# Performance work log

Hardware: AMD Instinct MI355X
Metric: run time of the kernel (lower is better)

Reference implementation:

```python
import jax, jax.numpy as jnp
import numpy as np

N_NODES = 50000
N_EDGES = 800000
D_IN = 128
H = 4
F = 16


def setup_inputs() -> dict:
    key = jax.random.key(0)
    k1, k2, k3, k4 = jax.random.split(key, 4)
    feat = jax.random.normal(k1, (N_NODES, D_IN), dtype=jnp.float32)
    W = jax.random.normal(k2, (D_IN, H * F), dtype=jnp.float32) / np.sqrt(D_IN)
    src = jax.random.randint(k3, (N_EDGES,), 0, N_NODES, dtype=jnp.int32)
    dst = jax.random.randint(k4, (N_EDGES,), 0, N_NODES, dtype=jnp.int32)
    return {"feat": feat, "W": W, "src": src, "dst": dst}


def reference(feat, W, src, dst):
    # Project: [N, D_in] @ [D_in, H*F] -> [N, H, F]
    ft = (feat @ W).reshape(N_NODES, H, F)
    # Per-edge dot-product scores, scaled: [E, H]
    e = jnp.einsum('ehf,ehf->eh', ft[src], ft[dst]) / np.sqrt(F).astype(np.float32)
    # Segment (per-destination) softmax over incoming edges
    seg_max = jax.ops.segment_max(e, dst, num_segments=N_NODES)  # [N, H]
    ex = jnp.exp(e - seg_max[dst])
    denom = jax.ops.segment_sum(ex, dst, num_segments=N_NODES)  # [N, H]
    sa = ex / denom[dst]  # [E, H]
    # Weighted scatter-sum of source features: [N, H, F]
    msgs = ft[src] * sa[:, :, None]
    out = jax.ops.segment_sum(msgs, dst, num_segments=N_NODES)
    return out
```

## Files before the change

kernel.cpp:

```cpp
#include <hip/hip_runtime.h>
#include <hip/hip_fp16.h>

#define N_NODES 50000
#define N_EDGES 800000
#define D_IN 128
#define HH 4
#define FF 16
#define HF 64
#define NBUCKETS 196
#define BCAP 4608
#define CHUNK 2048
#define NBIN_BLOCKS ((N_EDGES + CHUNK - 1) / CHUNK)
#define GEMM_BLOCKS ((N_NODES + 63) / 64)

struct __align__(8) Half4 { __half2 a, b; };

__global__ __launch_bounds__(256, 2) void gemm_kernel(const float* __restrict__ feat,
                                                      const float* __restrict__ W,
                                                      __half* __restrict__ fth) {
    __shared__ float As[64][132];
    __shared__ float Bs[D_IN][HF];

    {
        const float4* W4 = (const float4*)W;
        float4* B4 = (float4*)Bs;
#pragma unroll
        for (int i = 0; i < 8; ++i) {
            int idx = threadIdx.x + 256 * i;
            B4[idx] = W4[idx];
        }
    }
    {
        int row0 = blockIdx.x * 64;
        const float4* F4 = (const float4*)feat;
#pragma unroll
        for (int i = 0; i < 8; ++i) {
            int idx = threadIdx.x + 256 * i;
            int r = idx >> 5;
            int c4 = idx & 31;
            float4 v = make_float4(0.f, 0.f, 0.f, 0.f);
            int row = row0 + r;
            if (row < N_NODES) v = F4[(size_t)row * 32 + c4];
            *(float4*)&As[r][c4 * 4] = v;
        }
    }
    __syncthreads();

    const int tr = threadIdx.x >> 4;
    const int tc = threadIdx.x & 15;

    float acc[4][4] = {};
#pragma unroll 8
    for (int k = 0; k < D_IN; k += 4) {
        float av[4][4], bv[4][4];
#pragma unroll
        for (int i = 0; i < 4; ++i) {
            float4 a = *(const float4*)&As[tr * 4 + i][k];
            av[i][0] = a.x; av[i][1] = a.y; av[i][2] = a.z; av[i][3] = a.w;
        }
#pragma unroll
        for (int j = 0; j < 4; ++j) {
            float4 b = *(const float4*)&Bs[k + j][tc * 4];
            bv[j][0] = b.x; bv[j][1] = b.y; bv[j][2] = b.z; bv[j][3] = b.w;
        }
#pragma unroll
        for (int i = 0; i < 4; ++i)
#pragma unroll
            for (int j = 0; j < 4; ++j)
#pragma unroll
                for (int c = 0; c < 4; ++c)
                    acc[i][c] = fmaf(av[i][j], bv[j][c], acc[i][c]);
    }

    int row0 = blockIdx.x * 64;
#pragma unroll
    for (int i = 0; i < 4; ++i) {
        int row = row0 + tr * 4 + i;
        if (row < N_NODES) {
            Half4 h;
            h.a = __floats2half2_rn(acc[i][0], acc[i][1]);
            h.b = __floats2half2_rn(acc[i][2], acc[i][3]);
            *(Half4*)&fth[(size_t)row * HF + tc * 4] = h;
        }
    }
}

__global__ __launch_bounds__(256) void bin_kernel(const int* __restrict__ src,
                                                  const int* __restrict__ dst,
                                                  int* __restrict__ gcur,
                                                  int* __restrict__ recs) {
    __shared__ int hist[256];
    __shared__ int offs[256];
    __shared__ int cur[256];
    __shared__ int lrec[CHUNK];

    int tid = threadIdx.x;
    int e0 = blockIdx.x * CHUNK;
    int n = N_EDGES - e0; if (n > CHUNK) n = CHUNK;

    hist[tid] = 0;
    __syncthreads();

    int myrec[CHUNK / 256];
    int myb[CHUNK / 256];
#pragma unroll
    for (int k = 0; k < CHUNK / 256; ++k) {
        int idx = tid + k * 256;
        myb[k] = -1;
        if (idx < n) {
            int s = src[e0 + idx];
            int d = dst[e0 + idx];
            int b = d >> 8;
            myrec[k] = s | ((d & 255) << 16);
            myb[k] = b;
            atomicAdd(&hist[b], 1);
        }
    }
    __syncthreads();

    int val = hist[tid];
    offs[tid] = val;
    __syncthreads();
#pragma unroll
    for (int off = 1; off < 256; off <<= 1) {
        int t = (tid >= off) ? offs[tid - off] : 0;
        __syncthreads();
        offs[tid] += t;
        __syncthreads();
    }
    int excl = offs[tid] - val;
    __syncthreads();
    offs[tid] = excl;
    cur[tid] = excl;
    __syncthreads();

#pragma unroll
    for (int k = 0; k < CHUNK / 256; ++k) {
        if (myb[k] >= 0) {
            int p = atomicAdd(&cur[myb[k]], 1);
            lrec[p] = myrec[k];
        }
    }
    __syncthreads();

    if (tid < NBUCKETS) {
        int c = hist[tid];
        if (c > 0) {
            int g = atomicAdd(&gcur[tid], c);
            if (g + c > BCAP) c = (BCAP > g) ? (BCAP - g) : 0;
            int lo = offs[tid];
            int* dp = recs + (size_t)tid * BCAP + g;
            for (int i = 0; i < c; ++i) dp[i] = lrec[lo + i];
        }
    }
}

__global__ __launch_bounds__(256) void sort_kernel(const int* __restrict__ gcur,
                                                   const int* __restrict__ recs,
                                                   int* __restrict__ csr,
                                                   int* __restrict__ row_beg,
                                                   int* __restrict__ row_end) {
    __shared__ int lhist[256];
    __shared__ int loffs[256];
    __shared__ int lcur[256];
    __shared__ int sorted[BCAP];

    int tid = threadIdx.x;
    int b = blockIdx.x;
    int cnt = gcur[b]; if (cnt > BCAP) cnt = BCAP;
    const int* rp = recs + (size_t)b * BCAP;

    lhist[tid] = 0;
    __syncthreads();
    for (int i = tid; i < cnt; i += 256) atomicAdd(&lhist[rp[i] >> 16], 1);
    __syncthreads();

    int val = lhist[tid];
    loffs[tid] = val;
    __syncthreads();
#pragma unroll
    for (int off = 1; off < 256; off <<= 1) {
        int t = (tid >= off) ? loffs[tid - off] : 0;
        __syncthreads();
        loffs[tid] += t;
        __syncthreads();
    }
    int excl = loffs[tid] - val;
    __syncthreads();
    loffs[tid] = excl;
    lcur[tid] = excl;
    __syncthreads();

    for (int i = tid; i < cnt; i += 256) {
        int rec = rp[i];
        int p = atomicAdd(&lcur[rec >> 16], 1);
        sorted[p] = rec & 0xFFFF;
    }
    __syncthreads();

    int base = b * BCAP;
    for (int i = tid; i < cnt; i += 256) csr[base + i] = sorted[i];

    int node = b * 256 + tid;
    if (node < N_NODES) {
        row_beg[node] = base + excl;
        row_end[node] = base + excl + val;
    }
}

__global__ __launch_bounds__(256) void gather_kernel(const __half* __restrict__ fth,
                                                     const int* __restrict__ row_beg,
                                                     const int* __restrict__ row_end,
                                                     const int* __restrict__ csr,
                                                     float* __restrict__ out) {
    int node = __builtin_amdgcn_readfirstlane(blockIdx.x * 4 + (threadIdx.x >> 6));
    int lane = threadIdx.x & 63;

    int beg = row_beg[node];
    int end = row_end[node];

    float ftd = __half2float(fth[(size_t)node * HF + lane]);
    float acc = 0.0f, l = 0.0f;

    int i = beg;
    for (; i + 8 <= end; i += 8) {
        int s[8];
        float v[8];
#pragma unroll
        for (int j = 0; j < 8; ++j) s[j] = csr[i + j];
#pragma unroll
        for (int j = 0; j < 8; ++j) v[j] = __half2float(fth[(size_t)s[j] * HF + lane]);
#pragma unroll
        for (int j = 0; j < 8; ++j) {
            float p = ftd * v[j];
            p += __shfl_xor(p, 1, 64);
            p += __shfl_xor(p, 2, 64);
            p += __shfl_xor(p, 4, 64);
            p += __shfl_xor(p, 8, 64);
            float w = __expf(p * 0.25f);
            acc = fmaf(w, v[j], acc);
            l += w;
        }
    }
    for (; i + 4 <= end; i += 4) {
        int s[4];
        float v[4];
#pragma unroll
        for (int j = 0; j < 4; ++j) s[j] = csr[i + j];
#pragma unroll
        for (int j = 0; j < 4; ++j) v[j] = __half2float(fth[(size_t)s[j] * HF + lane]);
#pragma unroll
        for (int j = 0; j < 4; ++j) {
            float p = ftd * v[j];
            p += __shfl_xor(p, 1, 64);
            p += __shfl_xor(p, 2, 64);
            p += __shfl_xor(p, 4, 64);
            p += __shfl_xor(p, 8, 64);
            float w = __expf(p * 0.25f);
            acc = fmaf(w, v[j], acc);
            l += w;
        }
    }
    for (; i < end; ++i) {
        int s = csr[i];
        float v = __half2float(fth[(size_t)s * HF + lane]);
        float p = ftd * v;
        p += __shfl_xor(p, 1, 64);
        p += __shfl_xor(p, 2, 64);
        p += __shfl_xor(p, 4, 64);
        p += __shfl_xor(p, 8, 64);
        float w = __expf(p * 0.25f);
        acc = fmaf(w, v, acc);
        l += w;
    }

    out[(size_t)node * HF + lane] = (l > 0.0f) ? acc / l : 0.0f;
}

extern "C" void kernel_launch(void* const* d_in, const int* in_sizes, int n_in,
                              void* d_out, int out_size, void* d_ws, size_t ws_size,
                              hipStream_t stream) {
    const float* feat = (const float*)d_in[0];
    const float* W = (const float*)d_in[1];
    const int* src = (const int*)d_in[2];
    const int* dst = (const int*)d_in[3];
    float* out = (float*)d_out;

    __half* fth = (__half*)d_ws;
    int* recs = (int*)(fth + (size_t)N_NODES * HF);
    int* csr = recs + (size_t)NBUCKETS * BCAP;
    int* row_beg = csr + (size_t)NBUCKETS * BCAP;
    int* row_end = row_beg + N_NODES;
    int* gcur = row_end + N_NODES;

    hipMemsetAsync(gcur, 0, NBUCKETS * sizeof(int), stream);
    gemm_kernel<<<GEMM_BLOCKS, 256, 0, stream>>>(feat, W, fth);
    bin_kernel<<<NBIN_BLOCKS, 256, 0, stream>>>(src, dst, gcur, recs);
    sort_kernel<<<NBUCKETS, 256, 0, stream>>>(gcur, recs, csr, row_beg, row_end);
    gather_kernel<<<N_NODES * 64 / 256, 256, 0, stream>>>(fth, row_beg, row_end, csr, out);
}
```

Baseline: 157.1 us.

## Process two edges per wavefront in gather and coalesce bin/sort writes

The gather kernel now has each half-wave handle a different edge, with each lane holding a half2 of two features. This halves the shuffle reduction steps and the loop iterations per edge, and a cross-half shuffle combines the partial results at the end. The bin kernel reserves global bucket slots before the local scatter and writes records with all threads in a coalesced loop, instead of one thread per bucket copying serially. The sort kernel drops the shared staging array and scatters directly to csr, which cuts shared memory use but makes the global writes uncoalesced, and the dot products now use half-precision multiplies.

```diff
diff --git a/kernel.cpp b/kernel.cpp
--- a/kernel.cpp
+++ b/kernel.cpp
@@ -92,6 +92,7 @@
     __shared__ int hist[256];
     __shared__ int offs[256];
     __shared__ int cur[256];
+    __shared__ int gbase[256];
     __shared__ int lrec[CHUNK];
 
     int tid = threadIdx.x;
@@ -111,7 +112,7 @@
             int s = src[e0 + idx];
             int d = dst[e0 + idx];
             int b = d >> 8;
-            myrec[k] = s | ((d & 255) << 16);
+            myrec[k] = s | ((d & 255) << 16) | (b << 24);
             myb[k] = b;
             atomicAdd(&hist[b], 1);
         }
@@ -132,6 +133,7 @@
     __syncthreads();
     offs[tid] = excl;
     cur[tid] = excl;
+    if (tid < NBUCKETS && val > 0) gbase[tid] = atomicAdd(&gcur[tid], val);
     __syncthreads();
 
 #pragma unroll
@@ -143,15 +145,11 @@
     }
     __syncthreads();
 
-    if (tid < NBUCKETS) {
-        int c = hist[tid];
-        if (c > 0) {
-            int g = atomicAdd(&gcur[tid], c);
-            if (g + c > BCAP) c = (BCAP > g) ? (BCAP - g) : 0;
-            int lo = offs[tid];
-            int* dp = recs + (size_t)tid * BCAP + g;
-            for (int i = 0; i < c; ++i) dp[i] = lrec[lo + i];
-        }
+    for (int i = tid; i < n; i += 256) {
+        int r = lrec[i];
+        int b = (r >> 24) & 255;
+        int pos = gbase[b] + (i - offs[b]);
+        if (pos < BCAP) recs[(size_t)b * BCAP + pos] = r;
     }
 }
 
@@ -163,7 +161,6 @@
     __shared__ int lhist[256];
     __shared__ int loffs[256];
     __shared__ int lcur[256];
-    __shared__ int sorted[BCAP];
 
     int tid = threadIdx.x;
     int b = blockIdx.x;
@@ -172,7 +169,7 @@
 
     lhist[tid] = 0;
     __syncthreads();
-    for (int i = tid; i < cnt; i += 256) atomicAdd(&lhist[rp[i] >> 16], 1);
+    for (int i = tid; i < cnt; i += 256) atomicAdd(&lhist[(rp[i] >> 16) & 255], 1);
     __syncthreads();
 
     int val = lhist[tid];
@@ -187,19 +184,15 @@
     }
     int excl = loffs[tid] - val;
     __syncthreads();
-    loffs[tid] = excl;
     lcur[tid] = excl;
     __syncthreads();
 
+    int base = b * BCAP;
     for (int i = tid; i < cnt; i += 256) {
         int rec = rp[i];
-        int p = atomicAdd(&lcur[rec >> 16], 1);
-        sorted[p] = rec & 0xFFFF;
-    }
-    __syncthreads();
-
-    int base = b * BCAP;
-    for (int i = tid; i < cnt; i += 256) csr[base + i] = sorted[i];
+        int p = atomicAdd(&lcur[(rec >> 16) & 255], 1);
+        csr[base + p] = rec & 0xFFFF;
+    }
 
     int node = b * 256 + tid;
     if (node < N_NODES) {
@@ -215,66 +208,66 @@
                                                      float* __restrict__ out) {
     int node = __builtin_amdgcn_readfirstlane(blockIdx.x * 4 + (threadIdx.x >> 6));
     int lane = threadIdx.x & 63;
+    int hl = lane & 31;
+    bool hi = lane >= 32;
 
     int beg = row_beg[node];
     int end = row_end[node];
 
-    float ftd = __half2float(fth[(size_t)node * HF + lane]);
-    float acc = 0.0f, l = 0.0f;
+    __half2 ftd2 = *(const __half2*)&fth[(size_t)node * HF + 2 * hl];
+
+    float acc0 = 0.0f, acc1 = 0.0f, lsum = 0.0f;
 
     int i = beg;
-    for (; i + 8 <= end; i += 8) {
-        int s[8];
-        float v[8];
-#pragma unroll
-        for (int j = 0; j < 8; ++j) s[j] = csr[i + j];
-#pragma unroll
-        for (int j = 0; j < 8; ++j) v[j] = __half2float(fth[(size_t)s[j] * HF + lane]);
-#pragma unroll
-        for (int j = 0; j < 8; ++j) {
-            float p = ftd * v[j];
-            p += __shfl_xor(p, 1, 64);
-            p += __shfl_xor(p, 2, 64);
-            p += __shfl_xor(p, 4, 64);
-            p += __shfl_xor(p, 8, 64);
-            float w = __expf(p * 0.25f);
-            acc = fmaf(w, v[j], acc);
-            l += w;
-        }
-    }
     for (; i + 4 <= end; i += 4) {
-        int s[4];
-        float v[4];
-#pragma unroll
-        for (int j = 0; j < 4; ++j) s[j] = csr[i + j];
-#pragma unroll
-        for (int j = 0; j < 4; ++j) v[j] = __half2float(fth[(size_t)s[j] * HF + lane]);
-#pragma unroll
-        for (int j = 0; j < 4; ++j) {
-            float p = ftd * v[j];
-            p += __shfl_xor(p, 1, 64);
-            p += __shfl_xor(p, 2, 64);
-            p += __shfl_xor(p, 4, 64);
-            p += __shfl_xor(p, 8, 64);
-            float w = __expf(p * 0.25f);
-            acc = fmaf(w, v[j], acc);
-            l += w;
-        }
-    }
-    for (; i < end; ++i) {
-        int s = csr[i];
-        float v = __half2float(fth[(size_t)s * HF + lane]);
-        float p = ftd * v;
+        int sA0 = csr[i + 0], sB0 = csr[i + 1];
+        int sA1 = csr[i + 2], sB1 = csr[i + 3];
+        int s0 = hi ? sB0 : sA0;
+        int s1 = hi ? sB1 : sA1;
+        __half2 v20 = *(const __half2*)&fth[(size_t)s0 * HF + 2 * hl];
+        __half2 v21 = *(const __half2*)&fth[(size_t)s1 * HF + 2 * hl];
+
+        __half2 pr0 = __hmul2(ftd2, v20);
+        __half2 pr1 = __hmul2(ftd2, v21);
+        float p0 = __low2float(pr0) + __high2float(pr0);
+        float p1 = __low2float(pr1) + __high2float(pr1);
+        p0 += __shfl_xor(p0, 1, 64); p1 += __shfl_xor(p1, 1, 64);
+        p0 += __shfl_xor(p0, 2, 64); p1 += __shfl_xor(p1, 2, 64);
+        p0 += __shfl_xor(p0, 4, 64); p1 += __shfl_xor(p1, 4, 64);
+        float w0 = __expf(p0 * 0.25f);
+        float w1 = __expf(p1 * 0.25f);
+        acc0 = fmaf(w0, __low2float(v20), acc0);
+        acc1 = fmaf(w0, __high2float(v20), acc1);
+        acc0 = fmaf(w1, __low2float(v21), acc0);
+        acc1 = fmaf(w1, __high2float(v21), acc1);
+        lsum += w0 + w1;
+    }
+    for (; i < end; i += 2) {
+        bool hasB = (i + 1 < end);
+        int sA = csr[i];
+        int sB = hasB ? csr[i + 1] : sA;
+        int s = hi ? sB : sA;
+        __half2 v2 = *(const __half2*)&fth[(size_t)s * HF + 2 * hl];
+        __half2 pr = __hmul2(ftd2, v2);
+        float p = __low2float(pr) + __high2float(pr);
         p += __shfl_xor(p, 1, 64);
         p += __shfl_xor(p, 2, 64);
         p += __shfl_xor(p, 4, 64);
-        p += __shfl_xor(p, 8, 64);
         float w = __expf(p * 0.25f);
-        acc = fmaf(w, v, acc);
-        l += w;
-    }
-
-    out[(size_t)node * HF + lane] = (l > 0.0f) ? acc / l : 0.0f;
+        if (hi && !hasB) w = 0.0f;
+        acc0 = fmaf(w, __low2float(v2), acc0);
+        acc1 = fmaf(w, __high2float(v2), acc1);
+        lsum += w;
+    }
+
+    acc0 += __shfl_xor(acc0, 32, 64);
+    acc1 += __shfl_xor(acc1, 32, 64);
+    lsum += __shfl_xor(lsum, 32, 64);
+
+    if (!hi) {
+        float inv = (lsum > 0.0f) ? 1.0f / lsum : 0.0f;
+        *(float2*)&out[(size_t)node * HF + 2 * hl] = make_float2(acc0 * inv, acc1 * inv);
+    }
 }
 
 extern "C" void kernel_launch(void* const* d_in, const int* in_sizes, int n_in,
```

After: 149.1 us. -5.1%, faster.
